# Kernel optimization log

Measured on AMD Instinct MI355X. Metric: run time of the kernel, lower is better.

Reference implementation:

```python
import jax, jax.numpy as jnp
import numpy as np

N = 8192
SQUARE_SIZE = 10.0
NEIGHBOURHOOD = 1.0
THRESHOLD = 1.0
DECAY = 0.9


def setup_inputs() -> dict:
    key = jax.random.key(0)
    k1, k2, k3, k4 = jax.random.split(key, 4)
    # Random 2D topology on a square, as in SpikingLayer.__init__
    topo = jax.random.uniform(k1, (N, 2), dtype=jnp.float32) * SQUARE_SIZE
    # Pairwise squared distances without the [N,N,2] intermediate
    sq = jnp.sum(topo * topo, axis=1)  # [N]
    d2 = sq[:, None] + sq[None, :] - 2.0 * (topo @ topo.T)  # [N,N]
    mask = (d2 <= NEIGHBOURHOOD * NEIGHBOURHOOD).astype(jnp.float32)
    # Per-node weight rows, zeroed outside the neighbourhood radius
    W = jax.random.normal(k2, (N, N), dtype=jnp.float32) * mask
    # Random initial firing state (0/1) so dynamics are non-trivial
    f0 = (jax.random.uniform(k3, (N,)) > 0.5).astype(jnp.float32)
    v0 = jnp.zeros((N,), dtype=jnp.float32)
    x = jax.random.normal(k4, (N,), dtype=jnp.float32)  # unused, as in torch forward
    return {"W": W, "f0": f0, "v0": v0, "x": x, "num_steps": 64}


def reference(W, f0, v0, x, num_steps):
    # One scan step == one call to SpikingLayer.forward():
    #   node_x = W @ is_firing  (fused over all nodes)
    #   LIF update: v = decay*v + node_x; spike if v >= threshold; reset on spike
    def step(carry, _):
        v, f = carry
        u = W @ f                      # [N] weighted input from firing neighbours
        v = DECAY * v + u
        spike = v >= THRESHOLD         # bool [N]
        f_new = spike.astype(v.dtype)
        v = jnp.where(spike, 0.0, v)   # reset fired neurons
        return (v, f_new), f_new

    (_, _), firing_matrix = jax.lax.scan(step, (v0, f0), None, length=num_steps)
    return firing_matrix  # [num_steps, N], the accumulated firing_matrix
```

## Files before the change

kernel.cpp:

```cpp
#include <hip/hip_runtime.h>

#define NN 8192
#define STEPS 64
#define DECAYF 0.9f
#define THRESHF 1.0f
#define K_MAX 384
#define KITER 24

#define CBLOCKS 256
#define STHREADS 576

typedef unsigned long long u64;
typedef unsigned int u32;

__device__ __forceinline__ void pub_store(u64* p, u64 v) {
    __hip_atomic_store(p, v, __ATOMIC_RELAXED, __HIP_MEMORY_SCOPE_AGENT);
}
__device__ __forceinline__ u64 pub_load(const u64* p) {
    return __hip_atomic_load(p, __ATOMIC_RELAXED, __HIP_MEMORY_SCOPE_AGENT);
}

__global__ __launch_bounds__(256) void extract_ell(
        const float* __restrict__ W,
        u64* __restrict__ pk) {
    const int wave = threadIdx.x >> 6;
    const int lane = threadIdx.x & 63;
    const int row  = blockIdx.x * 4 + wave;
    const float4* wr4 = (const float4*)(W + (size_t)row * NN);
    u64* pr = pk + (size_t)row * K_MAX;
    const u64 lmask = (1ull << lane) - 1ull;

    int base = 0;
    for (int c4 = lane; c4 < NN / 4; c4 += 64) {
        float4 w = wr4[c4];
        const int col0 = c4 * 4;
        #pragma unroll
        for (int comp = 0; comp < 4; ++comp) {
            float val = (comp == 0) ? w.x : (comp == 1) ? w.y
                      : (comp == 2) ? w.z : w.w;
            u64 m = __ballot(val != 0.0f);
            if (val != 0.0f) {
                int idx = base + __popcll(m & lmask);
                if (idx < K_MAX)
                    pr[idx] = ((u64)(u32)(col0 + comp) << 32)
                            | (u64)__float_as_uint(val);
            }
            base += __popcll(m);
        }
    }
    const int cap = (base < K_MAX) ? base : K_MAX;
    for (int j = cap + lane; j < K_MAX; j += 64) pr[j] = 0ull;
}

__global__ __launch_bounds__(STHREADS) void spiking_steps(
        const u64* __restrict__ pk,
        const float* __restrict__ f0,
        const float* __restrict__ v0,
        float* __restrict__ out,
        u64* __restrict__ fdata) {
    __shared__ u32 lds_fbits[2][CBLOCKS];
    __shared__ u32 lds_spike[16];
    __shared__ int lds_flag;

    const int tid  = threadIdx.x;
    const int wave = tid >> 6;
    const int lane = tid & 63;
    const int bid  = blockIdx.x;

    if (tid < 16) lds_spike[tid] = 0;
    if (tid == 0) lds_flag = 0;

    if (wave == 0) {
        float f = (lane < 32) ? f0[bid * 32 + lane] : 0.0f;
        u64 m = __ballot(f != 0.0f);
        if (lane == 0)
            pub_store(&fdata[bid], (1ull << 32) | (u32)(m & 0xffffffffull));
    }
    __syncthreads();

    if (wave == 0) {
        for (int s = 0; s < STEPS; ++s) {
            const u64* slot = fdata + (size_t)(s & 1) * CBLOCKS;
            const u32 want = (u32)(s + 1);
            u64 w0, w1, w2, w3;
            for (;;) {
                w0 = pub_load(&slot[lane]);
                w1 = pub_load(&slot[lane + 64]);
                w2 = pub_load(&slot[lane + 128]);
                w3 = pub_load(&slot[lane + 192]);
                int ok = ((u32)(w0 >> 32) == want) & ((u32)(w1 >> 32) == want)
                       & ((u32)(w2 >> 32) == want) & ((u32)(w3 >> 32) == want);
                if (__all(ok)) break;
            }
            u32* fb = lds_fbits[s & 1];
            fb[lane]       = (u32)w0;
            fb[lane + 64]  = (u32)w1;
            fb[lane + 128] = (u32)w2;
            fb[lane + 192] = (u32)w3;
            if (lane == 0)
                __hip_atomic_store(&lds_flag, s + 1, __ATOMIC_RELEASE,
                                   __HIP_MEMORY_SCOPE_WORKGROUP);

            u32 myw;
            for (;;) {
                myw = (lane < 8)
                    ? __hip_atomic_load(&lds_spike[1 + lane], __ATOMIC_RELAXED,
                                        __HIP_MEMORY_SCOPE_WORKGROUP)
                    : (want << 8);
                if (__all((myw >> 8) == want)) break;
            }
            u32 bits = (lane < 8) ? ((myw & 0xFu) << (lane * 4)) : 0u;
            bits |= __shfl_xor(bits, 1, 64);
            bits |= __shfl_xor(bits, 2, 64);
            bits |= __shfl_xor(bits, 4, 64);
            if (lane == 0)
                pub_store(&fdata[(size_t)((s + 1) & 1) * CBLOCKS + bid],
                          ((u64)(u32)(s + 2) << 32) | bits);
        }
    } else {
        const int g    = wave - 1;
        const int rloc = g * 4 + (lane >> 4);
        const int row  = bid * 32 + rloc;
        const int l16  = lane & 15;

        u32 ecol[KITER]; float eval[KITER];
        const u64* pr = pk + (size_t)row * K_MAX;
        #pragma unroll
        for (int k = 0; k < KITER; ++k) {
            u64 p = pr[l16 + 16 * k];
            ecol[k] = (u32)(p >> 32);
            eval[k] = __uint_as_float((u32)p);
        }
        float vreg = v0[row];

        for (int s = 0; s < STEPS; ++s) {
            while (__hip_atomic_load(&lds_flag, __ATOMIC_ACQUIRE,
                                     __HIP_MEMORY_SCOPE_WORKGROUP) < s + 1)
                __builtin_amdgcn_s_sleep(2);
            const u32* fb = lds_fbits[s & 1];

            double acc = 0.0;
            #pragma unroll
            for (int k = 0; k < KITER; ++k) {
                u32 c = ecol[k];
                u32 w = fb[c >> 5];
                float sv = ((w >> (c & 31)) & 1u) ? eval[k] : 0.0f;
                acc += (double)sv;
            }
            #pragma unroll
            for (int m = 8; m >= 1; m >>= 1)
                acc += __shfl_xor(acc, m, 64);

            float u  = (float)acc;
            float vv = __fadd_rn(__fmul_rn(DECAYF, vreg), u);
            int fire = (vv >= THRESHF);
            vreg = fire ? 0.0f : vv;
            if (l16 == 0)
                out[(size_t)s * NN + row] = fire ? 1.0f : 0.0f;

            u64 bal = __ballot(fire);
            if (lane == 0) {
                u32 bits4 = ((u32)(bal       ) & 1u)
                          | (((u32)(bal >> 16) & 1u) << 1)
                          | (((u32)(bal >> 32) & 1u) << 2)
                          | (((u32)(bal >> 48) & 1u) << 3);
                __hip_atomic_store(&lds_spike[1 + g],
                                   ((u32)(s + 1) << 8) | bits4,
                                   __ATOMIC_RELAXED, __HIP_MEMORY_SCOPE_WORKGROUP);
            }
        }
    }
}

extern "C" void kernel_launch(void* const* d_in, const int* in_sizes, int n_in,
                              void* d_out, int out_size, void* d_ws, size_t ws_size,
                              hipStream_t stream) {
    const float* W  = (const float*)d_in[0];
    const float* f0 = (const float*)d_in[1];
    const float* v0 = (const float*)d_in[2];
    float* out = (float*)d_out;

    u64* pk    = (u64*)d_ws;
    u64* fdata = pk + (size_t)NN * K_MAX;

    extract_ell<<<dim3(NN / 4), dim3(256), 0, stream>>>(W, pk);
    spiking_steps<<<dim3(CBLOCKS), dim3(STHREADS), 0, stream>>>(
        pk, f0, v0, out, fdata);
}
```

Before: 607.1 us.

## Publish block spikes from last compute wave via LDS counter, drop coordinator spin

```diff
diff --git a/kernel.cpp b/kernel.cpp
--- a/kernel.cpp
+++ b/kernel.cpp
@@ -59,7 +59,8 @@
         float* __restrict__ out,
         u64* __restrict__ fdata) {
     __shared__ u32 lds_fbits[2][CBLOCKS];
-    __shared__ u32 lds_spike[16];
+    __shared__ u32 lds_spike[8];
+    __shared__ int lds_cnt[STEPS];
     __shared__ int lds_flag;
 
     const int tid  = threadIdx.x;
@@ -67,7 +68,7 @@
     const int lane = tid & 63;
     const int bid  = blockIdx.x;
 
-    if (tid < 16) lds_spike[tid] = 0;
+    if (tid < STEPS) lds_cnt[tid] = 0;
     if (tid == 0) lds_flag = 0;
 
     if (wave == 0) {
@@ -82,40 +83,24 @@
         for (int s = 0; s < STEPS; ++s) {
             const u64* slot = fdata + (size_t)(s & 1) * CBLOCKS;
             const u32 want = (u32)(s + 1);
-            u64 w0, w1, w2, w3;
+            u32* fb = lds_fbits[s & 1];
+            u32 pend = 0xFu;
             for (;;) {
-                w0 = pub_load(&slot[lane]);
-                w1 = pub_load(&slot[lane + 64]);
-                w2 = pub_load(&slot[lane + 128]);
-                w3 = pub_load(&slot[lane + 192]);
-                int ok = ((u32)(w0 >> 32) == want) & ((u32)(w1 >> 32) == want)
-                       & ((u32)(w2 >> 32) == want) & ((u32)(w3 >> 32) == want);
-                if (__all(ok)) break;
+                #pragma unroll
+                for (int k = 0; k < 4; ++k) {
+                    if ((pend >> k) & 1u) {
+                        u64 w = pub_load(&slot[lane + 64 * k]);
+                        if ((u32)(w >> 32) == want) {
+                            fb[lane + 64 * k] = (u32)w;
+                            pend &= ~(1u << k);
+                        }
+                    }
+                }
+                if (__all(pend == 0)) break;
             }
-            u32* fb = lds_fbits[s & 1];
-            fb[lane]       = (u32)w0;
-            fb[lane + 64]  = (u32)w1;
-            fb[lane + 128] = (u32)w2;
-            fb[lane + 192] = (u32)w3;
             if (lane == 0)
                 __hip_atomic_store(&lds_flag, s + 1, __ATOMIC_RELEASE,
                                    __HIP_MEMORY_SCOPE_WORKGROUP);
-
-            u32 myw;
-            for (;;) {
-                myw = (lane < 8)
-                    ? __hip_atomic_load(&lds_spike[1 + lane], __ATOMIC_RELAXED,
-                                        __HIP_MEMORY_SCOPE_WORKGROUP)
-                    : (want << 8);
-                if (__all((myw >> 8) == want)) break;
-            }
-            u32 bits = (lane < 8) ? ((myw & 0xFu) << (lane * 4)) : 0u;
-            bits |= __shfl_xor(bits, 1, 64);
-            bits |= __shfl_xor(bits, 2, 64);
-            bits |= __shfl_xor(bits, 4, 64);
-            if (lane == 0)
-                pub_store(&fdata[(size_t)((s + 1) & 1) * CBLOCKS + bid],
-                          ((u64)(u32)(s + 2) << 32) | bits);
         }
     } else {
         const int g    = wave - 1;
@@ -135,18 +120,20 @@
 
         for (int s = 0; s < STEPS; ++s) {
             while (__hip_atomic_load(&lds_flag, __ATOMIC_ACQUIRE,
-                                     __HIP_MEMORY_SCOPE_WORKGROUP) < s + 1)
-                __builtin_amdgcn_s_sleep(2);
+                                     __HIP_MEMORY_SCOPE_WORKGROUP) < s + 1) {}
             const u32* fb = lds_fbits[s & 1];
 
-            double acc = 0.0;
+            double a0 = 0.0, a1 = 0.0, a2 = 0.0;
             #pragma unroll
-            for (int k = 0; k < KITER; ++k) {
-                u32 c = ecol[k];
-                u32 w = fb[c >> 5];
-                float sv = ((w >> (c & 31)) & 1u) ? eval[k] : 0.0f;
-                acc += (double)sv;
+            for (int k = 0; k < KITER; k += 3) {
+                u32 c0 = ecol[k],     w0 = fb[c0 >> 5];
+                u32 c1 = ecol[k + 1], w1 = fb[c1 >> 5];
+                u32 c2 = ecol[k + 2], w2 = fb[c2 >> 5];
+                a0 += (double)(((w0 >> (c0 & 31)) & 1u) ? eval[k]     : 0.0f);
+                a1 += (double)(((w1 >> (c1 & 31)) & 1u) ? eval[k + 1] : 0.0f);
+                a2 += (double)(((w2 >> (c2 & 31)) & 1u) ? eval[k + 2] : 0.0f);
             }
+            double acc = (a0 + a1) + a2;
             #pragma unroll
             for (int m = 8; m >= 1; m >>= 1)
                 acc += __shfl_xor(acc, m, 64);
@@ -155,19 +142,32 @@
             float vv = __fadd_rn(__fmul_rn(DECAYF, vreg), u);
             int fire = (vv >= THRESHF);
             vreg = fire ? 0.0f : vv;
-            if (l16 == 0)
-                out[(size_t)s * NN + row] = fire ? 1.0f : 0.0f;
 
             u64 bal = __ballot(fire);
+            int old = -1;
             if (lane == 0) {
                 u32 bits4 = ((u32)(bal       ) & 1u)
                           | (((u32)(bal >> 16) & 1u) << 1)
                           | (((u32)(bal >> 32) & 1u) << 2)
                           | (((u32)(bal >> 48) & 1u) << 3);
-                __hip_atomic_store(&lds_spike[1 + g],
-                                   ((u32)(s + 1) << 8) | bits4,
-                                   __ATOMIC_RELAXED, __HIP_MEMORY_SCOPE_WORKGROUP);
+                __hip_atomic_store(&lds_spike[g], bits4, __ATOMIC_RELAXED,
+                                   __HIP_MEMORY_SCOPE_WORKGROUP);
+                old = __hip_atomic_fetch_add(&lds_cnt[s], 1, __ATOMIC_ACQ_REL,
+                                             __HIP_MEMORY_SCOPE_WORKGROUP);
             }
+            old = __shfl(old, 0, 64);
+            if (old == 7) {
+                u32 b = (lane < 8) ? ((lds_spike[lane] & 0xFu) << (4 * lane)) : 0u;
+                b |= __shfl_xor(b, 1, 64);
+                b |= __shfl_xor(b, 2, 64);
+                b |= __shfl_xor(b, 4, 64);
+                if (lane == 0)
+                    pub_store(&fdata[(size_t)((s + 1) & 1) * CBLOCKS + bid],
+                              ((u64)(u32)(s + 2) << 32) | b);
+            }
+
+            if (l16 == 0)
+                out[(size_t)s * NN + row] = fire ? 1.0f : 0.0f;
         }
     }
 }
```

After: 612.9 us. No clear change (+1.0%).
